# Kernel tuning notes

Hardware: AMD Instinct MI355X
Metric: run time of the kernel (lower is better)

The kernel has to match this reference:

```python
import jax, jax.numpy as jnp
import numpy as np

D_MODEL = 3072
N_HEADS = 24
MAX_LEN = 2048
ROPE_THETA = 10000.0
DH = D_MODEL // N_HEADS                  # 128
Q_PROJ = D_MODEL // 2                    # 1536
KV_PROJ = 2 * D_MODEL // 3               # 2048
NOPE = DH // 2                           # 64
ROPE = DH // 2                           # 64
EPS = 1e-5


def layernorm(x, w, b):
    m = jnp.mean(x, axis=-1, keepdims=True)
    v = jnp.mean(jnp.square(x - m), axis=-1, keepdims=True)
    return (x - m) / jnp.sqrt(v + EPS) * w + b


def rotate_half(x):
    h = x.shape[-1] // 2
    return jnp.concatenate([-x[..., h:], x[..., :h]], axis=-1)


def rope_tables(S):
    freqs = 1.0 / ROPE_THETA ** (jnp.arange(0, DH, 2, dtype=jnp.float32) / DH)  # [DH/2]
    emb = jnp.arange(S, dtype=jnp.float32)[:, None] * freqs[None, :]            # [S, DH/2]
    # torch: take first ROPE//2 freqs then .repeat(...,2) => tile along last axis
    cos = jnp.tile(jnp.cos(emb)[:, : ROPE // 2], (1, 2))  # [S, ROPE]
    sin = jnp.tile(jnp.sin(emb)[:, : ROPE // 2], (1, 2))
    return cos[None, None], sin[None, None]               # [1,1,S,ROPE]


def setup_inputs() -> dict:
    key = jax.random.key(0)
    ks = jax.random.split(key, 7)
    x = jax.random.normal(ks[0], (2, 2048, D_MODEL), dtype=jnp.float32)
    p = lambda k, shp: 0.01 * jax.random.normal(k, shp, dtype=jnp.float32)
    return {
        "x": x,
        "W_dq": p(ks[1], (D_MODEL, Q_PROJ)),
        "W_uq": p(ks[2], (Q_PROJ, D_MODEL)),
        "q_ln_w": jnp.ones((Q_PROJ,), jnp.float32),
        "q_ln_b": jnp.zeros((Q_PROJ,), jnp.float32),
        "W_dkv": p(ks[3], (D_MODEL, KV_PROJ + ROPE)),
        "W_ukv": p(ks[4], (KV_PROJ, D_MODEL + N_HEADS * NOPE)),
        "kv_ln_w": jnp.ones((KV_PROJ,), jnp.float32),
        "kv_ln_b": jnp.zeros((KV_PROJ,), jnp.float32),
        "W_o": p(ks[5], (D_MODEL, D_MODEL)),
    }


def reference(x, W_dq, W_uq, q_ln_w, q_ln_b, W_dkv, W_ukv, kv_ln_w, kv_ln_b, W_o):
    B, S, D = x.shape
    cos, sin = rope_tables(S)  # past_length=0, S_full=S

    # Q path: low-rank down/up projection
    cq = layernorm(x @ W_dq, q_ln_w, q_ln_b)          # [B,S,Q_PROJ]
    Q = (cq @ W_uq).reshape(B, S, N_HEADS, DH).transpose(0, 2, 1, 3)  # [B,H,S,DH]
    Q_nope, Q_rope = Q[..., :NOPE], Q[..., NOPE:]
    Q_rope = Q_rope * cos + rotate_half(Q_rope) * sin

    # KV path
    compressed_kv = x @ W_dkv                          # [B,S,KV_PROJ+ROPE]
    KV_lora = layernorm(compressed_kv[..., :KV_PROJ], kv_ln_w, kv_ln_b)
    K_rope = compressed_kv[..., KV_PROJ:]              # [B,S,ROPE]
    KV = (KV_lora @ W_ukv).reshape(B, S, N_HEADS, DH + NOPE).transpose(0, 2, 1, 3)
    K_nope, V = KV[..., :NOPE], KV[..., NOPE:]         # [B,H,S,NOPE], [B,H,S,DH]

    K_rope = K_rope[:, None]                           # [B,1,S,ROPE] shared head
    K_rope = K_rope * cos + rotate_half(K_rope) * sin

    q = jnp.concatenate([Q_nope, Q_rope], axis=-1)     # [B,H,S,DH]
    # k = cat(K_nope, K_rope broadcast over heads)
    k = jnp.concatenate([K_nope, jnp.broadcast_to(K_rope, (B, N_HEADS, S, ROPE))], axis=-1)

    scale = 1.0 / jnp.sqrt(jnp.float32(DH))
    scores = jnp.einsum("bhqd,bhkd->bhqk", q, k) * scale
    causal = jnp.tril(jnp.ones((S, S), dtype=bool))
    scores = jnp.where(causal[None, None], scores, jnp.float32(-jnp.inf))
    attn = jax.nn.softmax(scores, axis=-1)
    out = jnp.einsum("bhqk,bhkd->bhqd", attn, V)
    out = out.transpose(0, 2, 1, 3).reshape(B, S, D)
    out = out @ W_o.T
    return out, compressed_kv
```

## Files before the change

### kernel.cpp

```cpp
#include <hip/hip_runtime.h>

typedef unsigned short u16;
typedef __attribute__((ext_vector_type(8))) short short8;
typedef __attribute__((ext_vector_type(4))) float f32x4;

#define NROWS   4096
#define S_LEN   2048
#define NHEADS  24
#define DMODEL  3072
#define QPROJ   1536
#define KVPROJ  2048
#define CKV_W   2112
#define UKV_N   4608

__device__ __forceinline__ float bf2f(u16 v) {
    unsigned u = ((unsigned)v) << 16; float f; __builtin_memcpy(&f, &u, 4); return f;
}
__device__ __forceinline__ u16 f2bf(float f) {
    unsigned u; __builtin_memcpy(&u, &f, 4);
    u = (u + 0x7FFFu + ((u >> 16) & 1u)) >> 16; return (u16)u;
}
__device__ __forceinline__ u16 f2bf_trunc(float f) {
    unsigned u; __builtin_memcpy(&u, &f, 4);
    return (u16)(u >> 16);
}
__device__ __forceinline__ void async16(const u16* g, u16* l) {
    __builtin_amdgcn_global_load_lds((const __attribute__((address_space(1))) unsigned int*)g,
                                     (__attribute__((address_space(3))) unsigned int*)l,
                                     16, 0, 0);
}

__global__ void conv_bf16(const float* __restrict__ X, u16* __restrict__ Y, int n) {
    int i = (blockIdx.x * 256 + threadIdx.x) * 4;
    if (i >= n) return;
    float4 v = *(const float4*)(X + i);
    Y[i+0] = f2bf(v.x); Y[i+1] = f2bf(v.y); Y[i+2] = f2bf(v.z); Y[i+3] = f2bf(v.w);
}

__global__ void transpose_bf16(const float* __restrict__ W, u16* __restrict__ WT,
                               int K, int N, float scale) {
    __shared__ float t[32][33];
    int nb = blockIdx.x * 32, kb = blockIdx.y * 32;
    int c = threadIdx.x & 31, rq = threadIdx.x >> 5;
#pragma unroll
    for (int i = 0; i < 4; ++i) {
        int r = rq * 4 + i;
        t[r][c] = W[(size_t)(kb + r) * N + nb + c];
    }
    __syncthreads();
#pragma unroll
    for (int i = 0; i < 4; ++i) {
        int r = rq * 4 + i;
        WT[(size_t)(nb + r) * K + kb + c] = f2bf(t[c][r] * scale);
    }
}

__global__ __launch_bounds__(256) void ln_kernel(const float* __restrict__ X, int ldx,
                                                 const float* __restrict__ g,
                                                 const float* __restrict__ b,
                                                 u16* __restrict__ Y, int W) {
    int row = blockIdx.x;
    const float4* x4 = (const float4*)(X + (size_t)row * ldx);
    int W4 = W >> 2;
    float s = 0.f, s2 = 0.f;
    for (int i = threadIdx.x; i < W4; i += 256) {
        float4 v = x4[i];
        s += v.x + v.y + v.z + v.w;
        s2 += v.x * v.x + v.y * v.y + v.z * v.z + v.w * v.w;
    }
#pragma unroll
    for (int off = 32; off >= 1; off >>= 1) { s += __shfl_xor(s, off); s2 += __shfl_xor(s2, off); }
    __shared__ float red[8];
    int w = threadIdx.x >> 6;
    if ((threadIdx.x & 63) == 0) { red[w] = s; red[4 + w] = s2; }
    __syncthreads();
    s  = red[0] + red[1] + red[2] + red[3];
    s2 = red[4] + red[5] + red[6] + red[7];
    float mean = s / W;
    float var  = s2 / W - mean * mean;
    float rstd = rsqrtf(var + 1e-5f);
    const float4* g4 = (const float4*)g;
    const float4* b4 = (const float4*)b;
    u16* y = Y + (size_t)row * W;
    for (int i = threadIdx.x; i < W4; i += 256) {
        float4 v = x4[i], gg = g4[i], bb = b4[i];
        u16 o[4];
        o[0] = f2bf((v.x - mean) * rstd * gg.x + bb.x);
        o[1] = f2bf((v.y - mean) * rstd * gg.y + bb.y);
        o[2] = f2bf((v.z - mean) * rstd * gg.z + bb.z);
        o[3] = f2bf((v.w - mean) * rstd * gg.w + bb.w);
        *(ulong1*)&y[i * 4] = *(ulong1*)o;
    }
}

__global__ __launch_bounds__(256) void ln_bf16_kernel(const u16* __restrict__ X,
                                                      const float* __restrict__ g,
                                                      const float* __restrict__ b,
                                                      u16* __restrict__ Y, int W) {
    int row = blockIdx.x;
    const u16* x = X + (size_t)row * W;
    int W4 = W >> 2;
    float s = 0.f, s2 = 0.f;
    for (int i = threadIdx.x; i < W4; i += 256) {
        ushort4 v = *(const ushort4*)(x + i * 4);
        float a0 = bf2f(v.x), a1 = bf2f(v.y), a2 = bf2f(v.z), a3 = bf2f(v.w);
        s += a0 + a1 + a2 + a3;
        s2 += a0 * a0 + a1 * a1 + a2 * a2 + a3 * a3;
    }
#pragma unroll
    for (int off = 32; off >= 1; off >>= 1) { s += __shfl_xor(s, off); s2 += __shfl_xor(s2, off); }
    __shared__ float red[8];
    int w = threadIdx.x >> 6;
    if ((threadIdx.x & 63) == 0) { red[w] = s; red[4 + w] = s2; }
    __syncthreads();
    s  = red[0] + red[1] + red[2] + red[3];
    s2 = red[4] + red[5] + red[6] + red[7];
    float mean = s / W;
    float var  = s2 / W - mean * mean;
    float rstd = rsqrtf(var + 1e-5f);
    const float4* g4 = (const float4*)g;
    const float4* b4 = (const float4*)b;
    u16* y = Y + (size_t)row * W;
    for (int i = threadIdx.x; i < W4; i += 256) {
        ushort4 v = *(const ushort4*)(x + i * 4);
        float4 gg = g4[i], bb = b4[i];
        u16 o[4];
        o[0] = f2bf((bf2f(v.x) - mean) * rstd * gg.x + bb.x);
        o[1] = f2bf((bf2f(v.y) - mean) * rstd * gg.y + bb.y);
        o[2] = f2bf((bf2f(v.z) - mean) * rstd * gg.z + bb.z);
        o[3] = f2bf((bf2f(v.w) - mean) * rstd * gg.w + bb.w);
        *(ulong1*)&y[i * 4] = *(ulong1*)o;
    }
}

__global__ void rope_q_kernel(u16* __restrict__ Q) {
    int idx = blockIdx.x * 256 + threadIdx.x;
    int j = idx & 31; int t = idx >> 5; int h = t % NHEADS; int row = t / NHEADS;
    int s = row & (S_LEN - 1);
    float freq = __expf(-(float)j * (9.210340371976184f / 64.f));
    float ang = (float)s * freq;
    float c = cosf(ang), si = sinf(ang);
    u16* p = Q + (size_t)row * DMODEL + h * 128 + 64;
    float x1 = bf2f(p[j]), x2 = bf2f(p[j + 32]);
    p[j]      = f2bf(x1 * c - x2 * si);
    p[j + 32] = f2bf(x2 * c + x1 * si);
}

__global__ void rope_k_kernel(const float* __restrict__ ckv, u16* __restrict__ kr) {
    int idx = blockIdx.x * 256 + threadIdx.x;
    int j = idx & 31; int row = idx >> 5;
    int s = row & (S_LEN - 1);
    float freq = __expf(-(float)j * (9.210340371976184f / 64.f));
    float ang = (float)s * freq;
    float c = cosf(ang), si = sinf(ang);
    const float* src = ckv + (size_t)row * CKV_W + KVPROJ;
    float x1 = src[j], x2 = src[j + 32];
    kr[(size_t)row * 64 + j]      = f2bf(x1 * c - x2 * si);
    kr[(size_t)row * 64 + j + 32] = f2bf(x2 * c + x1 * si);
}

__global__ __launch_bounds__(256) void pack_k(const u16* __restrict__ KVb,
                                              const u16* __restrict__ kr,
                                              u16* __restrict__ Kp) {
    int bh = blockIdx.y, bb = bh / NHEADS, h = bh % NHEADS;
    int s0 = blockIdx.x * 64;
    int t = threadIdx.x;
    size_t base = (size_t)bb * S_LEN;
#pragma unroll
    for (int it = 0; it < 4; ++it) {
        int j = it * 256 + t;
        int r = j >> 4, cb = (j & 15) * 8;
        int s = s0 + r;
        uint4 v;
        if (cb < 64) v = *(const uint4*)&KVb[(base + s) * UKV_N + h * 192 + cb];
        else         v = *(const uint4*)&kr[(base + s) * 64 + (cb - 64)];
        *(uint4*)&Kp[((size_t)bh * S_LEN + s) * 128 + cb] = v;
    }
}

__global__ __launch_bounds__(256) void pack_v(const u16* __restrict__ KVb,
                                              u16* __restrict__ Vt) {
    __shared__ u16 tile[64][136];
    int bh = blockIdx.y, bb = bh / NHEADS, h = bh % NHEADS;
    int s0 = blockIdx.x * 64;
    int t = threadIdx.x;
    size_t base = (size_t)bb * S_LEN;
#pragma unroll
    for (int it = 0; it < 4; ++it) {
        int j = it * 256 + t;
        int r = j >> 4, cb = (j & 15) * 8;
        *(uint4*)&tile[r][cb] = *(const uint4*)&KVb[(base + s0 + r) * UKV_N + h * 192 + 64 + cb];
    }
    __syncthreads();
#pragma unroll
    for (int it = 0; it < 4; ++it) {
        int j = it * 256 + t;
        int d = j >> 3, sb = (j & 7) * 8;
        u16 tmp[8];
#pragma unroll
        for (int e = 0; e < 8; ++e) tmp[e] = tile[sb + e][d];
        *(uint4*)&Vt[((size_t)bh * 128 + d) * S_LEN + s0 + sb] = *(uint4*)tmp;
    }
}

template<bool OUT_BF16>
__global__ __launch_bounds__(256) void gemm_nt(const u16* __restrict__ A,
                                               const u16* __restrict__ B,
                                               void* __restrict__ Cv,
                                               int M, int N, int K, int nx) {
    __shared__ u16 a_lds[2][128][32];
    __shared__ u16 b_lds[2][128][32];
    int nwg = (int)gridDim.x;
    int bid = (int)blockIdx.x;
    int wg = (bid & 7) * (nwg >> 3) + (bid >> 3);
    int by = wg / nx, bx = wg - by * nx;
    int m0 = by * 128, n0 = bx * 128;
    int tid = threadIdx.x, lane = tid & 63, w = tid >> 6;
    int wm = w >> 1, wn = w & 1;
    int srow = lane >> 2;
    int kx = (lane >> 4) & 2;
    int scol = ((lane & 3) ^ kx) * 8;
    int r0 = w * 32 + srow, r1 = w * 32 + 16 + srow;
    const u16* A0 = A + (size_t)(m0 + r0) * K + scol;
    const u16* A1 = A + (size_t)(m0 + r1) * K + scol;
    int bn0 = n0 + r0; if (bn0 >= N) bn0 = N - 1;
    int bn1 = n0 + r1; if (bn1 >= N) bn1 = N - 1;
    const u16* B0 = B + (size_t)bn0 * K + scol;
    const u16* B1 = B + (size_t)bn1 * K + scol;
    char* aB = (char*)&a_lds[0][0][0];
    char* bB = (char*)&b_lds[0][0][0];
    int d0 = w * 2048, d1 = w * 2048 + 1024;
    int cb = ((lane >> 4) * 16) ^ ((lane & 8) << 2);

    f32x4 acc[4][4] = {};
    async16(A0, (u16*)(aB + d0)); async16(A1, (u16*)(aB + d1));
    async16(B0, (u16*)(bB + d0)); async16(B1, (u16*)(bB + d1));
    __syncthreads();
    int buf = 0;
    for (int kb = 0; kb < K; kb += 32) {
        if (kb + 32 < K) {
            int ob = (buf ^ 1) * 8192;
            async16(A0 + kb + 32, (u16*)(aB + ob + d0));
            async16(A1 + kb + 32, (u16*)(aB + ob + d1));
            async16(B0 + kb + 32, (u16*)(bB + ob + d0));
            async16(B1 + kb + 32, (u16*)(bB + ob + d1));
        }
        const char* ab = aB + buf * 8192;
        const char* bb = bB + buf * 8192;
        short8 af[4], bf[4];
#pragma unroll
        for (int i = 0; i < 4; ++i) {
            af[i] = *(const short8*)(ab + (wm * 64 + i * 16 + (lane & 15)) * 64 + cb);
            bf[i] = *(const short8*)(bb + (wn * 64 + i * 16 + (lane & 15)) * 64 + cb);
        }
#pragma unroll
        for (int i = 0; i < 4; ++i)
#pragma unroll
            for (int j = 0; j < 4; ++j)
                acc[i][j] = __builtin_amdgcn_mfma_f32_16x16x32_bf16(af[i], bf[j], acc[i][j], 0, 0, 0);
        __syncthreads();
        buf ^= 1;
    }
#pragma unroll
    for (int i = 0; i < 4; ++i) {
        int row = m0 + wm * 64 + i * 16 + ((lane >> 4) << 2);
#pragma unroll
        for (int j = 0; j < 4; ++j) {
            int col = n0 + wn * 64 + j * 16 + (lane & 15);
            if (col < N) {
#pragma unroll
                for (int r = 0; r < 4; ++r) {
                    if (OUT_BF16) ((u16*)Cv)[(size_t)(row + r) * N + col] = f2bf(acc[i][j][r]);
                    else          ((float*)Cv)[(size_t)(row + r) * N + col] = acc[i][j][r];
                }
            }
        }
    }
}

__global__ __launch_bounds__(256) void attn_kernel(const u16* __restrict__ Qb,
                                                   const u16* __restrict__ Kp,
                                                   const u16* __restrict__ Vt,
                                                   u16* __restrict__ AO) {
    __shared__ u16 k_lds[64][128];
    __shared__ u16 v_lds[128][64];
    __shared__ u16 p_lds[4][16][64];
    int bid = blockIdx.x;
    int jj = bid >> 3;
    int bh = (bid & 7) * 6 + (jj >> 4);
    int bx = jj & 15;
    int bb = bh / NHEADS, h = bh % NHEADS;
    int tid = threadIdx.x, lane = tid & 63, w = tid >> 6;
    size_t base = (size_t)bb * S_LEN;
    size_t bhS = (size_t)bh * S_LEN;

    const char* Kbyte = (const char*)Kp;
    const char* Vbyte = (const char*)Vt;
    char* kB = (char*)&k_lds[0][0];
    char* vB = (char*)&v_lds[0][0];
    char* pB = (char*)&p_lds[0][0][0] + w * 2048;
    size_t ksrc[4], vsrc[4];
    int kd[4];
#pragma unroll
    for (int is = 0; is < 4; ++is) {
        int j = is * 256 + tid;
        int r = j >> 4;
        int cbs = ((j & 15) * 16) ^ ((r & 7) << 4);
        ksrc[is] = (bhS + r) * 256 + cbs;
        int d = j >> 3;
        int kbs = (((j & 7) ^ (d & 7)) * 16);
        vsrc[is] = ((size_t)bh * 128 + d) * (S_LEN * 2) + kbs;
        kd[is] = (is * 256 + w * 64) * 16;
    }

    for (int seg = 0; seg < 2; ++seg) {
        int qx = seg == 0 ? (31 - bx) : bx;
        int q0 = qx * 64;

        short8 qf[4];
        {
            int qrow = q0 + w * 16 + (lane & 15);
            const u16* qp = Qb + (base + qrow) * DMODEL + h * 128 + ((lane >> 4) * 8);
#pragma unroll
            for (int ks = 0; ks < 4; ++ks) qf[ks] = *(const short8*)(qp + ks * 32);
        }

        f32x4 acc_o[8] = {};
        float m_run[4], l_run[4];
#pragma unroll
        for (int r = 0; r < 4; ++r) { m_run[r] = -1e30f; l_run[r] = 0.f; }

        int ntiles = qx + 1;
        for (int t = 0; t < ntiles; ++t) {
            size_t kv0 = (size_t)t * 64;
#pragma unroll
            for (int is = 0; is < 4; ++is)
                async16((const u16*)(Kbyte + ksrc[is] + kv0 * 256), (u16*)(kB + kd[is]));
#pragma unroll
            for (int is = 0; is < 4; ++is)
                async16((const u16*)(Vbyte + vsrc[is] + kv0 * 2), (u16*)(vB + kd[is]));
            __syncthreads();

            f32x4 sc[4];
            __builtin_amdgcn_s_setprio(1);
#pragma unroll
            for (int nb = 0; nb < 4; ++nb) {
                f32x4 a = {};
                int row = nb * 16 + (lane & 15);
                const char* kb_ = kB + row * 256;
                int x = (row & 7) << 4;
#pragma unroll
                for (int ks = 0; ks < 4; ++ks) {
                    short8 kf = *(const short8*)(kb_ + ((ks * 64 + (lane >> 4) * 16) ^ x));
                    a = __builtin_amdgcn_mfma_f32_16x16x32_bf16(qf[ks], kf, a, 0, 0, 0);
                }
                sc[nb] = a;
            }
            __builtin_amdgcn_s_setprio(0);

            if (t == qx) {
                int kvb = t * 64;
                int qg = q0 + w * 16 + ((lane >> 4) << 2);
#pragma unroll
                for (int nb = 0; nb < 4; ++nb) {
                    int kc = kvb + nb * 16 + (lane & 15);
#pragma unroll
                    for (int r = 0; r < 4; ++r)
                        if (kc > qg + r) sc[nb][r] = -1e30f;
                }
            }
            float rmax[4];
#pragma unroll
            for (int r = 0; r < 4; ++r)
                rmax[r] = fmaxf(fmaxf(sc[0][r], sc[1][r]), fmaxf(sc[2][r], sc[3][r]));
#pragma unroll
            for (int off = 1; off < 16; off <<= 1)
#pragma unroll
                for (int r = 0; r < 4; ++r) rmax[r] = fmaxf(rmax[r], __shfl_xor(rmax[r], off));

            bool ok = (rmax[0] <= m_run[0]) & (rmax[1] <= m_run[1]) &
                      (rmax[2] <= m_run[2]) & (rmax[3] <= m_run[3]);
            if (!__all(ok)) {
                float fac[4];
#pragma unroll
                for (int r = 0; r < 4; ++r) {
                    float mnew = fmaxf(m_run[r], rmax[r]);
                    fac[r] = __expf(m_run[r] - mnew);
                    m_run[r] = mnew;
                    l_run[r] *= fac[r];
                }
#pragma unroll
                for (int db = 0; db < 8; ++db)
#pragma unroll
                    for (int r = 0; r < 4; ++r) acc_o[db][r] *= fac[r];
            }
#pragma unroll
            for (int nb = 0; nb < 4; ++nb)
#pragma unroll
                for (int r = 0; r < 4; ++r) {
                    float p = __expf(sc[nb][r] - m_run[r]);
                    sc[nb][r] = p; l_run[r] += p;
                }

#pragma unroll
            for (int nb = 0; nb < 4; ++nb)
#pragma unroll
                for (int r = 0; r < 4; ++r) {
                    int row = ((lane >> 4) << 2) + r;
                    int cby = (nb * 32 + (lane & 15) * 2) ^ ((row & 7) << 4);
                    *(u16*)(pB + row * 128 + cby) = f2bf_trunc(sc[nb][r]);
                }
            __builtin_amdgcn_sched_barrier(0);
            __builtin_amdgcn_s_setprio(1);
#pragma unroll
            for (int ks = 0; ks < 2; ++ks) {
                int prow = lane & 15;
                short8 pf = *(const short8*)(pB + prow * 128 +
                                ((ks * 64 + (lane >> 4) * 16) ^ ((prow & 7) << 4)));
#pragma unroll
                for (int db = 0; db < 8; ++db) {
                    int row = db * 16 + (lane & 15);
                    const char* vb_ = vB + row * 128;
                    short8 vf = *(const short8*)(vb_ + ((ks * 64 + (lane >> 4) * 16) ^ ((row & 7) << 4)));
                    acc_o[db] = __builtin_amdgcn_mfma_f32_16x16x32_bf16(pf, vf, acc_o[db], 0, 0, 0);
                }
            }
            __builtin_amdgcn_s_setprio(0);
            __syncthreads();
        }

#pragma unroll
        for (int off = 1; off < 16; off <<= 1)
#pragma unroll
            for (int r = 0; r < 4; ++r) l_run[r] += __shfl_xor(l_run[r], off);

        int orow = q0 + w * 16 + ((lane >> 4) << 2);
#pragma unroll
        for (int db = 0; db < 8; ++db)
#pragma unroll
            for (int r = 0; r < 4; ++r) {
                float o = acc_o[db][r] / l_run[r];
                AO[(base + orow + r) * DMODEL + h * 128 + db * 16 + (lane & 15)] = f2bf(o);
            }
    }
}

extern "C" void kernel_launch(void* const* d_in, const int* in_sizes, int n_in,
                              void* d_out, int out_size, void* d_ws, size_t ws_size,
                              hipStream_t stream) {
    (void)in_sizes; (void)n_in; (void)out_size; (void)ws_size;
    const float* x      = (const float*)d_in[0];
    const float* W_dq   = (const float*)d_in[1];
    const float* W_uq   = (const float*)d_in[2];
    const float* q_ln_w = (const float*)d_in[3];
    const float* q_ln_b = (const float*)d_in[4];
    const float* W_dkv  = (const float*)d_in[5];
    const float* W_ukv  = (const float*)d_in[6];
    const float* kv_ln_w= (const float*)d_in[7];
    const float* kv_ln_b= (const float*)d_in[8];
    const float* W_o    = (const float*)d_in[9];

    float* out = (float*)d_out;
    float* ckv = out + (size_t)NROWS * DMODEL;

    char* ws = (char*)d_ws;
    const size_t OFF_WDQT  = 0;
    const size_t OFF_WUQT  = 9437184;
    const size_t OFF_WDKVT = 18874368;
    const size_t OFF_WUKVT = 31850496;
    const size_t OFF_WO    = 50724864;
    const size_t OFF_XB    = 69599232;
    const size_t OFF_QB    = 94765056;
    const size_t OFF_KVB   = 119930880;
    const size_t OFF_KR    = 157679616;
    const size_t OFF_SLABA = 158203904;
    const size_t OFF_SLABB = 183369728;
    const size_t OFF_KP    = 0;
    const size_t OFF_VT    = OFF_XB;

    u16* Wdq_t  = (u16*)(ws + OFF_WDQT);
    u16* Wuq_t  = (u16*)(ws + OFF_WUQT);
    u16* Wdkv_t = (u16*)(ws + OFF_WDKVT);
    u16* Wukv_t = (u16*)(ws + OFF_WUKVT);
    u16* Wo_b   = (u16*)(ws + OFF_WO);
    u16* xb     = (u16*)(ws + OFF_XB);
    u16* qb     = (u16*)(ws + OFF_QB);
    u16* KVb    = (u16*)(ws + OFF_KVB);
    u16* kr     = (u16*)(ws + OFF_KR);
    u16* t0b    = (u16*)(ws + OFF_SLABA);
    u16* ao     = (u16*)(ws + OFF_SLABA);
    u16* cq     = (u16*)(ws + OFF_SLABB);
    u16* kvl    = (u16*)(ws + OFF_SLABB);
    u16* Kp     = (u16*)(ws + OFF_KP);
    u16* Vt     = (u16*)(ws + OFF_VT);

    const float SCALE = 0.08838834764831845f;

    transpose_bf16<<<dim3(QPROJ / 32, DMODEL / 32), 256, 0, stream>>>(W_dq,  Wdq_t,  DMODEL, QPROJ, 1.0f);
    transpose_bf16<<<dim3(DMODEL / 32, QPROJ / 32), 256, 0, stream>>>(W_uq,  Wuq_t,  QPROJ, DMODEL, SCALE);
    transpose_bf16<<<dim3(CKV_W / 32, DMODEL / 32), 256, 0, stream>>>(W_dkv, Wdkv_t, DMODEL, CKV_W, 1.0f);
    transpose_bf16<<<dim3(UKV_N / 32, KVPROJ / 32), 256, 0, stream>>>(W_ukv, Wukv_t, KVPROJ, UKV_N, 1.0f);
    conv_bf16<<<9216, 256, 0, stream>>>(W_o, Wo_b, DMODEL * DMODEL);
    conv_bf16<<<12288, 256, 0, stream>>>(x, xb, NROWS * DMODEL);

    gemm_nt<true><<<(QPROJ / 128) * (NROWS / 128), 256, 0, stream>>>(xb, Wdq_t, t0b, NROWS, QPROJ, DMODEL, QPROJ / 128);
    ln_bf16_kernel<<<NROWS, 256, 0, stream>>>(t0b, q_ln_w, q_ln_b, cq, QPROJ);
    gemm_nt<true><<<(DMODEL / 128) * (NROWS / 128), 256, 0, stream>>>(cq, Wuq_t, qb, NROWS, DMODEL, QPROJ, DMODEL / 128);
    rope_q_kernel<<<12288, 256, 0, stream>>>(qb);

    gemm_nt<false><<<17 * (NROWS / 128), 256, 0, stream>>>(xb, Wdkv_t, ckv, NROWS, CKV_W, DMODEL, 17);
    ln_kernel<<<NROWS, 256, 0, stream>>>(ckv, CKV_W, kv_ln_w, kv_ln_b, kvl, KVPROJ);
    rope_k_kernel<<<512, 256, 0, stream>>>(ckv, kr);
    gemm_nt<true><<<(UKV_N / 128) * (NROWS / 128), 256, 0, stream>>>(kvl, Wukv_t, KVb, NROWS, UKV_N, KVPROJ, UKV_N / 128);

    pack_k<<<dim3(S_LEN / 64, 2 * NHEADS), 256, 0, stream>>>(KVb, kr, Kp);
    pack_v<<<dim3(S_LEN / 64, 2 * NHEADS), 256, 0, stream>>>(KVb, Vt);

    attn_kernel<<<768, 256, 0, stream>>>(qb, Kp, Vt, ao);

    gemm_nt<false><<<(DMODEL / 128) * (NROWS / 128), 256, 0, stream>>>(ao, Wo_b, out, NROWS, DMODEL, DMODEL, DMODEL / 128);
}
```

Measured before the change: 633.7 us.

## Fuse Q RoPE and K/V packing into GEMM epilogues, read K from split buffers

```diff
diff --git a/kernel.cpp b/kernel.cpp
--- a/kernel.cpp
+++ b/kernel.cpp
@@ -133,19 +133,6 @@
     }
 }
 
-__global__ void rope_q_kernel(u16* __restrict__ Q) {
-    int idx = blockIdx.x * 256 + threadIdx.x;
-    int j = idx & 31; int t = idx >> 5; int h = t % NHEADS; int row = t / NHEADS;
-    int s = row & (S_LEN - 1);
-    float freq = __expf(-(float)j * (9.210340371976184f / 64.f));
-    float ang = (float)s * freq;
-    float c = cosf(ang), si = sinf(ang);
-    u16* p = Q + (size_t)row * DMODEL + h * 128 + 64;
-    float x1 = bf2f(p[j]), x2 = bf2f(p[j + 32]);
-    p[j]      = f2bf(x1 * c - x2 * si);
-    p[j + 32] = f2bf(x2 * c + x1 * si);
-}
-
 __global__ void rope_k_kernel(const float* __restrict__ ckv, u16* __restrict__ kr) {
     int idx = blockIdx.x * 256 + threadIdx.x;
     int j = idx & 31; int row = idx >> 5;
@@ -159,54 +146,12 @@
     kr[(size_t)row * 64 + j + 32] = f2bf(x2 * c + x1 * si);
 }
 
-__global__ __launch_bounds__(256) void pack_k(const u16* __restrict__ KVb,
-                                              const u16* __restrict__ kr,
-                                              u16* __restrict__ Kp) {
-    int bh = blockIdx.y, bb = bh / NHEADS, h = bh % NHEADS;
-    int s0 = blockIdx.x * 64;
-    int t = threadIdx.x;
-    size_t base = (size_t)bb * S_LEN;
-#pragma unroll
-    for (int it = 0; it < 4; ++it) {
-        int j = it * 256 + t;
-        int r = j >> 4, cb = (j & 15) * 8;
-        int s = s0 + r;
-        uint4 v;
-        if (cb < 64) v = *(const uint4*)&KVb[(base + s) * UKV_N + h * 192 + cb];
-        else         v = *(const uint4*)&kr[(base + s) * 64 + (cb - 64)];
-        *(uint4*)&Kp[((size_t)bh * S_LEN + s) * 128 + cb] = v;
-    }
-}
-
-__global__ __launch_bounds__(256) void pack_v(const u16* __restrict__ KVb,
-                                              u16* __restrict__ Vt) {
-    __shared__ u16 tile[64][136];
-    int bh = blockIdx.y, bb = bh / NHEADS, h = bh % NHEADS;
-    int s0 = blockIdx.x * 64;
-    int t = threadIdx.x;
-    size_t base = (size_t)bb * S_LEN;
-#pragma unroll
-    for (int it = 0; it < 4; ++it) {
-        int j = it * 256 + t;
-        int r = j >> 4, cb = (j & 15) * 8;
-        *(uint4*)&tile[r][cb] = *(const uint4*)&KVb[(base + s0 + r) * UKV_N + h * 192 + 64 + cb];
-    }
-    __syncthreads();
-#pragma unroll
-    for (int it = 0; it < 4; ++it) {
-        int j = it * 256 + t;
-        int d = j >> 3, sb = (j & 7) * 8;
-        u16 tmp[8];
-#pragma unroll
-        for (int e = 0; e < 8; ++e) tmp[e] = tile[sb + e][d];
-        *(uint4*)&Vt[((size_t)bh * 128 + d) * S_LEN + s0 + sb] = *(uint4*)tmp;
-    }
-}
-
-template<bool OUT_BF16>
+template<int MODE>
 __global__ __launch_bounds__(256) void gemm_nt(const u16* __restrict__ A,
                                                const u16* __restrict__ B,
                                                void* __restrict__ Cv,
+                                               u16* __restrict__ Kn,
+                                               u16* __restrict__ Vt,
                                                int M, int N, int K, int nx) {
     __shared__ u16 a_lds[2][128][32];
     __shared__ u16 b_lds[2][128][32];
@@ -261,6 +206,57 @@
         __syncthreads();
         buf ^= 1;
     }
+
+    if (MODE == 2 && wn == 1) {
+#pragma unroll
+        for (int i = 0; i < 4; ++i) {
+            int rowg = m0 + wm * 64 + i * 16 + ((lane >> 4) << 2);
+#pragma unroll
+            for (int j = 0; j < 2; ++j) {
+                int jf = j * 16 + (lane & 15);
+                float freq = __expf(-(float)jf * (9.210340371976184f / 64.f));
+#pragma unroll
+                for (int r = 0; r < 4; ++r) {
+                    int s = (rowg + r) & (S_LEN - 1);
+                    float ang = (float)s * freq;
+                    float cs, sn;
+                    __sincosf(ang, &sn, &cs);
+                    float x1 = acc[i][j][r], x2 = acc[i][j + 2][r];
+                    acc[i][j][r]     = x1 * cs - x2 * sn;
+                    acc[i][j + 2][r] = x2 * cs + x1 * sn;
+                }
+            }
+        }
+    }
+
+    if (MODE == 3) {
+#pragma unroll
+        for (int i = 0; i < 4; ++i) {
+            int rowg = m0 + wm * 64 + i * 16 + ((lane >> 4) << 2);
+            int bb = rowg >> 11;
+            int s0 = rowg & (S_LEN - 1);
+#pragma unroll
+            for (int j = 0; j < 4; ++j) {
+                int colbase = n0 + wn * 64 + j * 16;
+                int h = colbase / 192;
+                int c = colbase - h * 192 + (lane & 15);
+                int bh = bb * NHEADS + h;
+                if (c < 64) {
+#pragma unroll
+                    for (int r = 0; r < 4; ++r)
+                        Kn[((size_t)bh * S_LEN + s0 + r) * 64 + c] = f2bf(acc[i][j][r]);
+                } else {
+                    size_t vb = ((size_t)bh * 128 + (c - 64)) * S_LEN + s0;
+                    u16 o[4];
+#pragma unroll
+                    for (int r = 0; r < 4; ++r) o[r] = f2bf(acc[i][j][r]);
+                    *(ushort4*)&Vt[vb] = *(ushort4*)o;
+                }
+            }
+        }
+        return;
+    }
+
 #pragma unroll
     for (int i = 0; i < 4; ++i) {
         int row = m0 + wm * 64 + i * 16 + ((lane >> 4) << 2);
@@ -270,8 +266,8 @@
             if (col < N) {
 #pragma unroll
                 for (int r = 0; r < 4; ++r) {
-                    if (OUT_BF16) ((u16*)Cv)[(size_t)(row + r) * N + col] = f2bf(acc[i][j][r]);
-                    else          ((float*)Cv)[(size_t)(row + r) * N + col] = acc[i][j][r];
+                    if (MODE != 0) ((u16*)Cv)[(size_t)(row + r) * N + col] = f2bf(acc[i][j][r]);
+                    else           ((float*)Cv)[(size_t)(row + r) * N + col] = acc[i][j][r];
                 }
             }
         }
@@ -279,7 +275,8 @@
 }
 
 __global__ __launch_bounds__(256) void attn_kernel(const u16* __restrict__ Qb,
-                                                   const u16* __restrict__ Kp,
+                                                   const u16* __restrict__ Kn,
+                                                   const u16* __restrict__ kr_,
                                                    const u16* __restrict__ Vt,
                                                    u16* __restrict__ AO) {
     __shared__ u16 k_lds[64][128];
@@ -294,19 +291,21 @@
     size_t base = (size_t)bb * S_LEN;
     size_t bhS = (size_t)bh * S_LEN;
 
-    const char* Kbyte = (const char*)Kp;
     const char* Vbyte = (const char*)Vt;
     char* kB = (char*)&k_lds[0][0];
     char* vB = (char*)&v_lds[0][0];
     char* pB = (char*)&p_lds[0][0][0] + w * 2048;
-    size_t ksrc[4], vsrc[4];
+    const char* psrc[4];
+    size_t vsrc[4];
     int kd[4];
 #pragma unroll
     for (int is = 0; is < 4; ++is) {
         int j = is * 256 + tid;
         int r = j >> 4;
-        int cbs = ((j & 15) * 16) ^ ((r & 7) << 4);
-        ksrc[is] = (bhS + r) * 256 + cbs;
+        int p = j & 15;
+        int lq = p ^ (r & 7);
+        if (lq < 8) psrc[is] = (const char*)Kn  + (bhS  + r) * 128 + lq * 16;
+        else        psrc[is] = (const char*)kr_ + (base + r) * 128 + (lq - 8) * 16;
         int d = j >> 3;
         int kbs = (((j & 7) ^ (d & 7)) * 16);
         vsrc[is] = ((size_t)bh * 128 + d) * (S_LEN * 2) + kbs;
@@ -335,7 +334,7 @@
             size_t kv0 = (size_t)t * 64;
 #pragma unroll
             for (int is = 0; is < 4; ++is)
-                async16((const u16*)(Kbyte + ksrc[is] + kv0 * 256), (u16*)(kB + kd[is]));
+                async16((const u16*)(psrc[is] + kv0 * 128), (u16*)(kB + kd[is]));
 #pragma unroll
             for (int is = 0; is < 4; ++is)
                 async16((const u16*)(Vbyte + vsrc[is] + kv0 * 2), (u16*)(vB + kd[is]));
@@ -471,11 +470,10 @@
     const size_t OFF_WO    = 50724864;
     const size_t OFF_XB    = 69599232;
     const size_t OFF_QB    = 94765056;
-    const size_t OFF_KVB   = 119930880;
+    const size_t OFF_KN    = 119930880;
     const size_t OFF_KR    = 157679616;
     const size_t OFF_SLABA = 158203904;
     const size_t OFF_SLABB = 183369728;
-    const size_t OFF_KP    = 0;
     const size_t OFF_VT    = OFF_XB;
 
     u16* Wdq_t  = (u16*)(ws + OFF_WDQT);
@@ -485,13 +483,12 @@
     u16* Wo_b   = (u16*)(ws + OFF_WO);
     u16* xb     = (u16*)(ws + OFF_XB);
     u16* qb     = (u16*)(ws + OFF_QB);
-    u16* KVb    = (u16*)(ws + OFF_KVB);
+    u16* Kn     = (u16*)(ws + OFF_KN);
     u16* kr     = (u16*)(ws + OFF_KR);
     u16* t0b    = (u16*)(ws + OFF_SLABA);
     u16* ao     = (u16*)(ws + OFF_SLABA);
     u16* cq     = (u16*)(ws + OFF_SLABB);
     u16* kvl    = (u16*)(ws + OFF_SLABB);
-    u16* Kp     = (u16*)(ws + OFF_KP);
     u16* Vt     = (u16*)(ws + OFF_VT);
 
     const float SCALE = 0.08838834764831845f;
@@ -503,20 +500,16 @@
     conv_bf16<<<9216, 256, 0, stream>>>(W_o, Wo_b, DMODEL * DMODEL);
     conv_bf16<<<12288, 256, 0, stream>>>(x, xb, NROWS * DMODEL);
 
-    gemm_nt<true><<<(QPROJ / 128) * (NROWS / 128), 256, 0, stream>>>(xb, Wdq_t, t0b, NROWS, QPROJ, DMODEL, QPROJ / 128);
+    gemm_nt<1><<<(QPROJ / 128) * (NROWS / 128), 256, 0, stream>>>(xb, Wdq_t, t0b, nullptr, nullptr, NROWS, QPROJ, DMODEL, QPROJ / 128);
     ln_bf16_kernel<<<NROWS, 256, 0, stream>>>(t0b, q_ln_w, q_ln_b, cq, QPROJ);
-    gemm_nt<true><<<(DMODEL / 128) * (NROWS / 128), 256, 0, stream>>>(cq, Wuq_t, qb, NROWS, DMODEL, QPROJ, DMODEL / 128);
-    rope_q_kernel<<<12288, 256, 0, stream>>>(qb);
-
-    gemm_nt<false><<<17 * (NROWS / 128), 256, 0, stream>>>(xb, Wdkv_t, ckv, NROWS, CKV_W, DMODEL, 17);
+    gemm_nt<2><<<(DMODEL / 128) * (NROWS / 128), 256, 0, stream>>>(cq, Wuq_t, qb, nullptr, nullptr, NROWS, DMODEL, QPROJ, DMODEL / 128);
+
+    gemm_nt<0><<<17 * (NROWS / 128), 256, 0, stream>>>(xb, Wdkv_t, ckv, nullptr, nullptr, NROWS, CKV_W, DMODEL, 17);
     ln_kernel<<<NROWS, 256, 0, stream>>>(ckv, CKV_W, kv_ln_w, kv_ln_b, kvl, KVPROJ);
     rope_k_kernel<<<512, 256, 0, stream>>>(ckv, kr);
-    gemm_nt<true><<<(UKV_N / 128) * (NROWS / 128), 256, 0, stream>>>(kvl, Wukv_t, KVb, NROWS, UKV_N, KVPROJ, UKV_N / 128);
-
-    pack_k<<<dim3(S_LEN / 64, 2 * NHEADS), 256, 0, stream>>>(KVb, kr, Kp);
-    pack_v<<<dim3(S_LEN / 64, 2 * NHEADS), 256, 0, stream>>>(KVb, Vt);
-
-    attn_kernel<<<768, 256, 0, stream>>>(qb, Kp, Vt, ao);
-
-    gemm_nt<false><<<(DMODEL / 128) * (NROWS / 128), 256, 0, stream>>>(ao, Wo_b, out, NROWS, DMODEL, DMODEL, DMODEL / 128);
-}
+    gemm_nt<3><<<(UKV_N / 128) * (NROWS / 128), 256, 0, stream>>>(kvl, Wukv_t, nullptr, Kn, Vt, NROWS, UKV_N, KVPROJ, UKV_N / 128);
+
+    attn_kernel<<<768, 256, 0, stream>>>(qb, Kn, kr, Vt, ao);
+
+    gemm_nt<0><<<(DMODEL / 128) * (NROWS / 128), 256, 0, stream>>>(ao, Wo_b, out, nullptr, nullptr, NROWS, DMODEL, DMODEL, DMODEL / 128);
+}
```

Result: faster. 615.0 us (median of 2 runs) (-2.9%).
